# Performance work log

Hardware: AMD Instinct MI355X
Metric: run time of the kernel (lower is better)

The kernel has to match this reference:

```python
import jax, jax.numpy as jnp
import numpy as np


def gcn_conv(x, src, dst, norm, W, b, n_nodes):
    # PyG GCNConv: out[dst] = sum_edges norm * (x @ W)[src] + b
    h = x @ W                      # [N, F_out]
    msg = h[src] * norm[:, None]   # [E', F_out] gather + scale
    out = jax.ops.segment_sum(msg, dst, num_segments=n_nodes)
    return out + b


def _gcn_norm(edge_index, n_nodes):
    # add self loops, compute symmetric normalization deg^-1/2[src]*deg^-1/2[dst]
    loop = jnp.arange(n_nodes, dtype=edge_index.dtype)
    src = jnp.concatenate([edge_index[0], loop])
    dst = jnp.concatenate([edge_index[1], loop])
    deg = jnp.zeros((n_nodes,), jnp.float32).at[dst].add(1.0)
    dinv = jnp.where(deg > 0, jax.lax.rsqrt(deg), 0.0)
    norm = dinv[src] * dinv[dst]
    return src, dst, norm


def setup_inputs() -> dict:
    key = jax.random.key(0)
    ks = jax.random.split(key, 5)
    N, E, C_in, C_out = 50000, 800000, 128, 32
    H = 2 * C_out
    x = jax.random.normal(ks[0], (N, C_in), jnp.float32)
    edge_index = jax.random.randint(ks[1], (2, E), 0, N, jnp.int64)
    s1 = 1.0 / np.sqrt(C_in)
    s2 = 1.0 / np.sqrt(H)
    W1 = jax.random.uniform(ks[2], (C_in, H), jnp.float32, -s1, s1)
    b1 = jnp.zeros((H,), jnp.float32)
    W_mu = jax.random.uniform(ks[3], (H, C_out), jnp.float32, -s2, s2)
    b_mu = jnp.zeros((C_out,), jnp.float32)
    W_ls = jax.random.uniform(ks[4], (H, C_out), jnp.float32, -s2, s2)
    b_ls = jnp.zeros((C_out,), jnp.float32)
    return {"x": x, "edge_index": edge_index, "W1": W1, "b1": b1,
            "W_mu": W_mu, "b_mu": b_mu, "W_ls": W_ls, "b_ls": b_ls}


def reference(x, edge_index, W1, b1, W_mu, b_mu, W_ls, b_ls):
    n_nodes = x.shape[0]
    src, dst, norm = _gcn_norm(edge_index, n_nodes)
    h = jax.nn.relu(gcn_conv(x, src, dst, norm, W1, b1, n_nodes))
    mu = gcn_conv(h, src, dst, norm, W_mu, b_mu, n_nodes)
    logstd = gcn_conv(h, src, dst, norm, W_ls, b_ls, n_nodes)
    return mu, logstd
```

## Files before the change

kernel.cpp:

```cpp
#include <hip/hip_runtime.h>
#include <hip/hip_fp16.h>
#include <math.h>


typedef unsigned int uint;
typedef unsigned short ushort;
typedef __attribute__((ext_vector_type(8))) short short8;
typedef __attribute__((ext_vector_type(4))) float f32x4;

__device__ __forceinline__ ushort f2bf(float x) {
    uint u = __float_as_uint(x);
    u += 0x7fffu + ((u >> 16) & 1u);
    return (ushort)(u >> 16);
}
__device__ __forceinline__ float bf2f(ushort h) {
    return __uint_as_float((uint)h << 16);
}

__global__ __launch_bounds__(256) void k_hist(
        const int* __restrict__ dst, int* __restrict__ bcount, int E) {
    __shared__ int h[256];
    const int tid = threadIdx.x;
    h[tid] = 0;
    __syncthreads();
    const int base = blockIdx.x * 2048;
    #pragma unroll
    for (int k = 0; k < 8; ++k) {
        int i = base + k * 256 + tid;
        if (i < E) {
            int d = __builtin_nontemporal_load(dst + i);
            atomicAdd(&h[d >> 8], 1);
        }
    }
    __syncthreads();
    if (h[tid]) atomicAdd(&bcount[tid], h[tid]);
}

__global__ __launch_bounds__(256) void k_scatterA(
        const int* __restrict__ src, const int* __restrict__ dst,
        const int* __restrict__ bcount, int* __restrict__ bcursor,
        uint* __restrict__ recs, int E) {
    __shared__ int h[256];
    __shared__ int p[256];
    __shared__ int rb[256];
    const int tid = threadIdx.x;
    h[tid] = 0;
    __syncthreads();
    const int base = blockIdx.x * 2048;
    uint rec[8]; int rk[8];
    #pragma unroll
    for (int k = 0; k < 8; ++k) {
        int i = base + k * 256 + tid;
        if (i < E) {
            int s = __builtin_nontemporal_load(src + i);
            int d = __builtin_nontemporal_load(dst + i);
            int b = d >> 8;
            rec[k] = (uint)s | ((uint)(d & 255) << 16) | ((uint)b << 24);
            rk[k] = atomicAdd(&h[b], 1);
        }
    }
    int v = bcount[tid];
    p[tid] = v;
    __syncthreads();
    #pragma unroll
    for (int off = 1; off < 256; off <<= 1) {
        int x = (tid >= off) ? p[tid - off] : 0;
        __syncthreads();
        p[tid] += x;
        __syncthreads();
    }
    const int excl = p[tid] - v;
    const int hv = h[tid];
    rb[tid] = excl + (hv ? atomicAdd(&bcursor[tid], hv) : 0);
    __syncthreads();
    #pragma unroll
    for (int k = 0; k < 8; ++k) {
        int i = base + k * 256 + tid;
        if (i < E) recs[rb[rec[k] >> 24] + rk[k]] = rec[k];
    }
}

__global__ __launch_bounds__(256, 4) void k_phaseB(
        const uint* __restrict__ recs, const int* __restrict__ bcount,
        int* __restrict__ row_ptr, float* __restrict__ dinv,
        ushort* __restrict__ edges, int N, int E, int NBUCK) {
    __shared__ int h[256];
    __shared__ int p[256];
    __shared__ uint rstage[8192];
    const int tid = threadIdx.x;
    const int bx  = blockIdx.x;
    int v = bcount[tid];
    p[tid] = v;
    h[tid] = 0;
    __syncthreads();
    #pragma unroll
    for (int off = 1; off < 256; off <<= 1) {
        int x = (tid >= off) ? p[tid - off] : 0;
        __syncthreads();
        p[tid] += x;
        __syncthreads();
    }
    const int cnt = bcount[bx];
    const int bs  = p[bx] - cnt;
    const bool stg = (cnt <= 8192);
    for (int i = tid; i < cnt; i += 256) {
        uint r = recs[bs + i];
        if (stg) rstage[i] = r;
        atomicAdd(&h[(r >> 16) & 255], 1);
    }
    __syncthreads();
    v = h[tid];
    p[tid] = v;
    __syncthreads();
    #pragma unroll
    for (int off = 1; off < 256; off <<= 1) {
        int x = (tid >= off) ? p[tid - off] : 0;
        __syncthreads();
        p[tid] += x;
        __syncthreads();
    }
    const int excl = p[tid] - v;
    const int node = bx * 256 + tid;
    if (node < N) {
        row_ptr[node] = bs + excl;
        dinv[node] = rsqrtf((float)(v + 1));
    }
    if (bx == NBUCK - 1 && tid == 0) row_ptr[N] = E;
    h[tid] = excl;
    __syncthreads();
    for (int i = tid; i < cnt; i += 256) {
        uint r = stg ? rstage[i] : recs[bs + i];
        int pos = atomicAdd(&h[(r >> 16) & 255], 1);
        edges[bs + pos] = (ushort)(r & 0xffffu);
    }
}

__global__ __launch_bounds__(256, 4) void k_gemm(
        const float* __restrict__ x, const float* __restrict__ W1,
        const float* __restrict__ dinv, ushort* __restrict__ hp, int N) {
    const int tid = threadIdx.x;
    const int w = tid >> 6, l = tid & 63;
    const int m = l & 15, q = l >> 4;
    const int row0 = blockIdx.x * 64 + w * 16;
    const size_t arow = (size_t)min(row0 + m, N - 1);
    f32x4 acc0 = {0.f, 0.f, 0.f, 0.f}, acc1 = acc0, acc2 = acc0, acc3 = acc0;
    #pragma unroll
    for (int kc = 0; kc < 4; ++kc) {
        const int kofs = kc * 32 + q * 8;
        const float4* xr = (const float4*)(x + arow * 128 + kofs);
        float4 xa = xr[0], xb = xr[1];
        short8 a;
        a[0] = (short)f2bf(xa.x); a[1] = (short)f2bf(xa.y);
        a[2] = (short)f2bf(xa.z); a[3] = (short)f2bf(xa.w);
        a[4] = (short)f2bf(xb.x); a[5] = (short)f2bf(xb.y);
        a[6] = (short)f2bf(xb.z); a[7] = (short)f2bf(xb.w);
        short8 b0, b1, b2, b3;
        #pragma unroll
        for (int i = 0; i < 8; ++i) {
            const float* wk = W1 + (size_t)(kofs + i) * 64 + m;
            b0[i] = (short)f2bf(wk[0]);
            b1[i] = (short)f2bf(wk[16]);
            b2[i] = (short)f2bf(wk[32]);
            b3[i] = (short)f2bf(wk[48]);
        }
        acc0 = __builtin_amdgcn_mfma_f32_16x16x32_bf16(a, b0, acc0, 0, 0, 0);
        acc1 = __builtin_amdgcn_mfma_f32_16x16x32_bf16(a, b1, acc1, 0, 0, 0);
        acc2 = __builtin_amdgcn_mfma_f32_16x16x32_bf16(a, b2, acc2, 0, 0, 0);
        acc3 = __builtin_amdgcn_mfma_f32_16x16x32_bf16(a, b3, acc3, 0, 0, 0);
    }
    #pragma unroll
    for (int r = 0; r < 4; ++r) {
        int row = row0 + q * 4 + r;
        if (row >= N) continue;
        float dv = dinv[row];
        ushort* hr = hp + (size_t)row * 64 + m;
        hr[0]  = f2bf(acc0[r] * dv);
        hr[16] = f2bf(acc1[r] * dv);
        hr[32] = f2bf(acc2[r] * dv);
        hr[48] = f2bf(acc3[r] * dv);
    }
}

__device__ __forceinline__ f32x4 gather_grp(
        const uint* __restrict__ hp, const ushort* __restrict__ edges,
        int beg, int end, int E, int ql) {
    f32x4 acc = {0.f, 0.f, 0.f, 0.f};
    const int len = end - beg;
    int base = beg;
    for (int c = len >> 4; c > 0; --c, base += 16) {
        int mrec = (int)edges[base + ql];
        #pragma unroll
        for (int half = 0; half < 2; ++half) {
            #pragma unroll
            for (int i = 0; i < 8; ++i) {
                int r = __shfl(mrec, half * 8 + i, 16);
                uint2 v = *(const uint2*)(hp + (size_t)r * 32 + 2 * ql);
                f32x4 vf;
                vf.x = __uint_as_float(v.x << 16);
                vf.y = __uint_as_float(v.x & 0xffff0000u);
                vf.z = __uint_as_float(v.y << 16);
                vf.w = __uint_as_float(v.y & 0xffff0000u);
                acc = acc + vf;
            }
        }
    }
    const int rem = len & 15;
    if (rem) {
        int mrec = (int)edges[min(base + ql, E - 1)];
        for (int i = 0; i < rem; i += 4) {
            #pragma unroll
            for (int j = 0; j < 4; ++j) {
                int e = i + j;
                int r = __shfl(mrec, min(e, rem - 1), 16);
                uint2 v = *(const uint2*)(hp + (size_t)r * 32 + 2 * ql);
                if (e >= rem) { v.x = 0u; v.y = 0u; }
                f32x4 vf;
                vf.x = __uint_as_float(v.x << 16);
                vf.y = __uint_as_float(v.x & 0xffff0000u);
                vf.z = __uint_as_float(v.y << 16);
                vf.w = __uint_as_float(v.y & 0xffff0000u);
                acc = acc + vf;
            }
        }
    }
    return acc;
}

__global__ __launch_bounds__(256, 8) void k_gather1(
        const uint* __restrict__ hp, const int* __restrict__ row_ptr,
        const ushort* __restrict__ edges, const float* __restrict__ dinv,
        const float* __restrict__ b1, uint* __restrict__ ho, int N, int E) {
    const int lane = threadIdx.x & 63;
    const int ql = lane & 15;
    const int n = blockIdx.x * 16 + ((threadIdx.x >> 6) << 2) + (lane >> 4);
    const int nc = min(n, N - 1);
    const int beg = row_ptr[nc], end = row_ptr[nc + 1];
    f32x4 acc = gather_grp(hp, edges, beg, end, E, ql);
    const float dv = dinv[nc];
    const uint2 sv = *(const uint2*)(hp + (size_t)nc * 32 + 2 * ql);
    const float4 b = ((const float4*)b1)[ql];
    float s0 = acc.x + bf2f((ushort)sv.x);
    float s1 = acc.y + bf2f((ushort)(sv.x >> 16));
    float s2 = acc.z + bf2f((ushort)sv.y);
    float s3 = acc.w + bf2f((ushort)(sv.y >> 16));
    float h0 = fmaxf(fmaf(dv, s0, b.x), 0.f) * dv;
    float h1 = fmaxf(fmaf(dv, s1, b.y), 0.f) * dv;
    float h2 = fmaxf(fmaf(dv, s2, b.z), 0.f) * dv;
    float h3 = fmaxf(fmaf(dv, s3, b.w), 0.f) * dv;
    if (n < N) {
        uint2 o;
        o.x = (uint)f2bf(h0) | ((uint)f2bf(h1) << 16);
        o.y = (uint)f2bf(h2) | ((uint)f2bf(h3) << 16);
        *(uint2*)(ho + (size_t)n * 32 + 2 * ql) = o;
    }
}

__global__ __launch_bounds__(256, 8) void k_gather2(
        const uint* __restrict__ hp, const int* __restrict__ row_ptr,
        const ushort* __restrict__ edges, const float* __restrict__ dinv,
        const float* __restrict__ Wmu, const float* __restrict__ Wls,
        const float* __restrict__ bmu, const float* __restrict__ bls,
        float* __restrict__ out, int N, int E) {
    __shared__ __align__(16) float hs[4][4][64];
    const int lane = threadIdx.x & 63;
    const int ql = lane & 15, grp = lane >> 4;
    const int w = threadIdx.x >> 6;
    const int n = blockIdx.x * 16 + (w << 2) + grp;
    const int nc = min(n, N - 1);
    const int beg = row_ptr[nc], end = row_ptr[nc + 1];
    f32x4 acc = gather_grp(hp, edges, beg, end, E, ql);
    const float dv = dinv[nc];
    const uint2 sv = *(const uint2*)(hp + (size_t)nc * 32 + 2 * ql);
    float4 g;
    g.x = dv * (acc.x + bf2f((ushort)sv.x));
    g.y = dv * (acc.y + bf2f((ushort)(sv.x >> 16)));
    g.z = dv * (acc.z + bf2f((ushort)sv.y));
    g.w = dv * (acc.w + bf2f((ushort)(sv.y >> 16)));
    *(float4*)&hs[w][grp][4 * ql] = g;
    const float* Wsel = (lane < 32) ? (Wmu + lane) : (Wls + (lane - 32));
    const float bias  = (lane < 32) ? bmu[lane] : bls[lane - 32];
    float c0 = 0.f, c1 = 0.f, c2 = 0.f, c3 = 0.f;
    #pragma unroll 4
    for (int k = 0; k < 64; ++k) {
        float wv = Wsel[k * 32];
        c0 = fmaf(hs[w][0][k], wv, c0);
        c1 = fmaf(hs[w][1][k], wv, c1);
        c2 = fmaf(hs[w][2][k], wv, c2);
        c3 = fmaf(hs[w][3][k], wv, c3);
    }
    const int n0 = blockIdx.x * 16 + (w << 2);
    float cs[4] = {c0, c1, c2, c3};
    #pragma unroll
    for (int gg = 0; gg < 4; ++gg) {
        int nn = n0 + gg;
        if (nn >= N) break;
        float t = cs[gg] + bias;
        if (lane < 32) out[(size_t)nn * 32 + lane] = t;
        else           out[(size_t)N * 32 + (size_t)nn * 32 + (lane - 32)] = t;
    }
}

extern "C" void kernel_launch(void* const* d_in, const int* in_sizes, int n_in,
                              void* d_out, int out_size, void* d_ws, size_t ws_size,
                              hipStream_t stream) {
    const float* x   = (const float*)d_in[0];
    const int*   ei  = (const int*)d_in[1];
    const float* W1  = (const float*)d_in[2];
    const float* b1  = (const float*)d_in[3];
    const float* Wmu = (const float*)d_in[4];
    const float* bmu = (const float*)d_in[5];
    const float* Wls = (const float*)d_in[6];
    const float* bls = (const float*)d_in[7];
    float* out = (float*)d_out;

    const int N = in_sizes[0] / 128;
    const int E = in_sizes[1] / 2;
    const int* src = ei;
    const int* dst = ei + E;
    const int HB    = (E + 2047) / 2048;
    const int NBUCK = (N + 255) / 256;
    const int GB    = (N + 63) / 64;
    const int NG    = (N + 15) / 16;

    char* w = (char*)d_ws;
    auto carve = [&](size_t bytes) { char* p = w; w += (bytes + 1023) & ~(size_t)1023; return p; };
    int*    bcount  = (int*)   carve(512 * 4);
    int*    bcursor = bcount + 256;
    uint*   recs    = (uint*)  carve((size_t)E * 4);
    int*    row_ptr = (int*)   carve((size_t)(N + 1) * 4);
    float*  dinv    = (float*) carve((size_t)N * 4);
    ushort* edges   = (ushort*)carve((size_t)E * 2);
    ushort* h_pre   = (ushort*)carve((size_t)N * 64 * 2);
    ushort* h_mid   = (ushort*)carve((size_t)N * 64 * 2);

    hipMemsetAsync(bcount, 0, 512 * 4, stream);
    k_hist    <<<HB, 256, 0, stream>>>(dst, bcount, E);
    k_scatterA<<<HB, 256, 0, stream>>>(src, dst, bcount, bcursor, recs, E);
    k_phaseB  <<<NBUCK, 256, 0, stream>>>(recs, bcount, row_ptr, dinv, edges, N, E, NBUCK);
    k_gemm    <<<GB, 256, 0, stream>>>(x, W1, dinv, h_pre, N);
    k_gather1 <<<NG, 256, 0, stream>>>((const uint*)h_pre, row_ptr, edges, dinv,
                                       b1, (uint*)h_mid, N, E);
    k_gather2 <<<NG, 256, 0, stream>>>((const uint*)h_mid, row_ptr, edges, dinv,
                                       Wmu, Wls, bmu, bls, out, N, E);
}
```

Before: 188.8 us.

## Stage bf16 W1 in LDS for GEMM and gather with 8-lane groups using 16B loads

The GEMM kernel now converts W1 to bf16 once per block into a transposed shared-memory tile and reads B fragments as 16-byte LDS loads, instead of issuing many strided scalar global loads with per-element conversion. The gather kernels switch from 16 lanes per node with 8-byte loads to 8 lanes per node with 16-byte loads, so each wave handles 8 nodes and each block 32. Edge batches are 8 wide, with a masked tail of up to 7. The aim is fewer memory instructions per neighbour row and more nodes in flight, at the cost of more registers (occupancy hint lowered to 6) and extra GEMM prologue work.

```diff
diff --git a/kernel.cpp b/kernel.cpp
--- a/kernel.cpp
+++ b/kernel.cpp
@@ -138,7 +138,19 @@
 __global__ __launch_bounds__(256, 4) void k_gemm(
         const float* __restrict__ x, const float* __restrict__ W1,
         const float* __restrict__ dinv, ushort* __restrict__ hp, int N) {
+    __shared__ ushort Wt[64][136];
     const int tid = threadIdx.x;
+    #pragma unroll
+    for (int it = 0; it < 8; ++it) {
+        int idx = (it * 256 + tid) * 4;
+        int k = idx >> 6, c = idx & 63;
+        float4 wv = *(const float4*)(W1 + idx);
+        Wt[c + 0][k] = f2bf(wv.x);
+        Wt[c + 1][k] = f2bf(wv.y);
+        Wt[c + 2][k] = f2bf(wv.z);
+        Wt[c + 3][k] = f2bf(wv.w);
+    }
+    __syncthreads();
     const int w = tid >> 6, l = tid & 63;
     const int m = l & 15, q = l >> 4;
     const int row0 = blockIdx.x * 64 + w * 16;
@@ -154,15 +166,10 @@
         a[2] = (short)f2bf(xa.z); a[3] = (short)f2bf(xa.w);
         a[4] = (short)f2bf(xb.x); a[5] = (short)f2bf(xb.y);
         a[6] = (short)f2bf(xb.z); a[7] = (short)f2bf(xb.w);
-        short8 b0, b1, b2, b3;
-        #pragma unroll
-        for (int i = 0; i < 8; ++i) {
-            const float* wk = W1 + (size_t)(kofs + i) * 64 + m;
-            b0[i] = (short)f2bf(wk[0]);
-            b1[i] = (short)f2bf(wk[16]);
-            b2[i] = (short)f2bf(wk[32]);
-            b3[i] = (short)f2bf(wk[48]);
-        }
+        short8 b0 = *(const short8*)&Wt[m][kofs];
+        short8 b1 = *(const short8*)&Wt[m + 16][kofs];
+        short8 b2 = *(const short8*)&Wt[m + 32][kofs];
+        short8 b3 = *(const short8*)&Wt[m + 48][kofs];
         acc0 = __builtin_amdgcn_mfma_f32_16x16x32_bf16(a, b0, acc0, 0, 0, 0);
         acc1 = __builtin_amdgcn_mfma_f32_16x16x32_bf16(a, b1, acc1, 0, 0, 0);
         acc2 = __builtin_amdgcn_mfma_f32_16x16x32_bf16(a, b2, acc2, 0, 0, 0);
@@ -181,122 +188,137 @@
     }
 }
 
-__device__ __forceinline__ f32x4 gather_grp(
+__device__ __forceinline__ void gather_grp8(
         const uint* __restrict__ hp, const ushort* __restrict__ edges,
-        int beg, int end, int E, int ql) {
-    f32x4 acc = {0.f, 0.f, 0.f, 0.f};
-    const int len = end - beg;
-    int base = beg;
-    for (int c = len >> 4; c > 0; --c, base += 16) {
-        int mrec = (int)edges[base + ql];
-        #pragma unroll
-        for (int half = 0; half < 2; ++half) {
+        int beg, int end, int E, int sl, float4& a0, float4& a1) {
+    for (int base = beg; base < end; base += 8) {
+        const int mrec = (int)edges[min(base + sl, E - 1)];
+        const int cnt = end - base;
+        if (cnt >= 8) {
             #pragma unroll
             for (int i = 0; i < 8; ++i) {
-                int r = __shfl(mrec, half * 8 + i, 16);
-                uint2 v = *(const uint2*)(hp + (size_t)r * 32 + 2 * ql);
-                f32x4 vf;
-                vf.x = __uint_as_float(v.x << 16);
-                vf.y = __uint_as_float(v.x & 0xffff0000u);
-                vf.z = __uint_as_float(v.y << 16);
-                vf.w = __uint_as_float(v.y & 0xffff0000u);
-                acc = acc + vf;
+                const int r = __shfl(mrec, i, 8);
+                const uint4 v = *(const uint4*)(hp + (size_t)r * 32 + 4 * sl);
+                a0.x += __uint_as_float(v.x << 16);
+                a0.y += __uint_as_float(v.x & 0xffff0000u);
+                a0.z += __uint_as_float(v.y << 16);
+                a0.w += __uint_as_float(v.y & 0xffff0000u);
+                a1.x += __uint_as_float(v.z << 16);
+                a1.y += __uint_as_float(v.z & 0xffff0000u);
+                a1.z += __uint_as_float(v.w << 16);
+                a1.w += __uint_as_float(v.w & 0xffff0000u);
             }
-        }
-    }
-    const int rem = len & 15;
-    if (rem) {
-        int mrec = (int)edges[min(base + ql, E - 1)];
-        for (int i = 0; i < rem; i += 4) {
+        } else {
             #pragma unroll
-            for (int j = 0; j < 4; ++j) {
-                int e = i + j;
-                int r = __shfl(mrec, min(e, rem - 1), 16);
-                uint2 v = *(const uint2*)(hp + (size_t)r * 32 + 2 * ql);
-                if (e >= rem) { v.x = 0u; v.y = 0u; }
-                f32x4 vf;
-                vf.x = __uint_as_float(v.x << 16);
-                vf.y = __uint_as_float(v.x & 0xffff0000u);
-                vf.z = __uint_as_float(v.y << 16);
-                vf.w = __uint_as_float(v.y & 0xffff0000u);
-                acc = acc + vf;
+            for (int i = 0; i < 7; ++i) {
+                const int r = __shfl(mrec, min(i, cnt - 1), 8);
+                uint4 v = *(const uint4*)(hp + (size_t)r * 32 + 4 * sl);
+                if (i >= cnt) { v.x = 0u; v.y = 0u; v.z = 0u; v.w = 0u; }
+                a0.x += __uint_as_float(v.x << 16);
+                a0.y += __uint_as_float(v.x & 0xffff0000u);
+                a0.z += __uint_as_float(v.y << 16);
+                a0.w += __uint_as_float(v.y & 0xffff0000u);
+                a1.x += __uint_as_float(v.z << 16);
+                a1.y += __uint_as_float(v.z & 0xffff0000u);
+                a1.z += __uint_as_float(v.w << 16);
+                a1.w += __uint_as_float(v.w & 0xffff0000u);
             }
         }
     }
-    return acc;
-}
-
-__global__ __launch_bounds__(256, 8) void k_gather1(
+}
+
+__global__ __launch_bounds__(256, 6) void k_gather1(
         const uint* __restrict__ hp, const int* __restrict__ row_ptr,
         const ushort* __restrict__ edges, const float* __restrict__ dinv,
         const float* __restrict__ b1, uint* __restrict__ ho, int N, int E) {
     const int lane = threadIdx.x & 63;
-    const int ql = lane & 15;
-    const int n = blockIdx.x * 16 + ((threadIdx.x >> 6) << 2) + (lane >> 4);
+    const int sl = lane & 7;
+    const int n = blockIdx.x * 32 + ((threadIdx.x >> 6) << 3) + (lane >> 3);
     const int nc = min(n, N - 1);
     const int beg = row_ptr[nc], end = row_ptr[nc + 1];
-    f32x4 acc = gather_grp(hp, edges, beg, end, E, ql);
+    float4 a0 = {0.f, 0.f, 0.f, 0.f}, a1 = a0;
+    gather_grp8(hp, edges, beg, end, E, sl, a0, a1);
     const float dv = dinv[nc];
-    const uint2 sv = *(const uint2*)(hp + (size_t)nc * 32 + 2 * ql);
-    const float4 b = ((const float4*)b1)[ql];
-    float s0 = acc.x + bf2f((ushort)sv.x);
-    float s1 = acc.y + bf2f((ushort)(sv.x >> 16));
-    float s2 = acc.z + bf2f((ushort)sv.y);
-    float s3 = acc.w + bf2f((ushort)(sv.y >> 16));
-    float h0 = fmaxf(fmaf(dv, s0, b.x), 0.f) * dv;
-    float h1 = fmaxf(fmaf(dv, s1, b.y), 0.f) * dv;
-    float h2 = fmaxf(fmaf(dv, s2, b.z), 0.f) * dv;
-    float h3 = fmaxf(fmaf(dv, s3, b.w), 0.f) * dv;
+    const uint4 sv = *(const uint4*)(hp + (size_t)nc * 32 + 4 * sl);
+    const float4 bA = ((const float4*)b1)[2 * sl];
+    const float4 bB = ((const float4*)b1)[2 * sl + 1];
+    float s0 = a0.x + bf2f((ushort)sv.x);
+    float s1 = a0.y + bf2f((ushort)(sv.x >> 16));
+    float s2 = a0.z + bf2f((ushort)sv.y);
+    float s3 = a0.w + bf2f((ushort)(sv.y >> 16));
+    float s4 = a1.x + bf2f((ushort)sv.z);
+    float s5 = a1.y + bf2f((ushort)(sv.z >> 16));
+    float s6 = a1.z + bf2f((ushort)sv.w);
+    float s7 = a1.w + bf2f((ushort)(sv.w >> 16));
+    float h0 = fmaxf(fmaf(dv, s0, bA.x), 0.f) * dv;
+    float h1 = fmaxf(fmaf(dv, s1, bA.y), 0.f) * dv;
+    float h2 = fmaxf(fmaf(dv, s2, bA.z), 0.f) * dv;
+    float h3 = fmaxf(fmaf(dv, s3, bA.w), 0.f) * dv;
+    float h4 = fmaxf(fmaf(dv, s4, bB.x), 0.f) * dv;
+    float h5 = fmaxf(fmaf(dv, s5, bB.y), 0.f) * dv;
+    float h6 = fmaxf(fmaf(dv, s6, bB.z), 0.f) * dv;
+    float h7 = fmaxf(fmaf(dv, s7, bB.w), 0.f) * dv;
     if (n < N) {
-        uint2 o;
+        uint4 o;
         o.x = (uint)f2bf(h0) | ((uint)f2bf(h1) << 16);
         o.y = (uint)f2bf(h2) | ((uint)f2bf(h3) << 16);
-        *(uint2*)(ho + (size_t)n * 32 + 2 * ql) = o;
-    }
-}
-
-__global__ __launch_bounds__(256, 8) void k_gather2(
+        o.z = (uint)f2bf(h4) | ((uint)f2bf(h5) << 16);
+        o.w = (uint)f2bf(h6) | ((uint)f2bf(h7) << 16);
+        *(uint4*)(ho + (size_t)n * 32 + 4 * sl) = o;
+    }
+}
+
+__global__ __launch_bounds__(256, 6) void k_gather2(
         const uint* __restrict__ hp, const int* __restrict__ row_ptr,
         const ushort* __restrict__ edges, const float* __restrict__ dinv,
         const float* __restrict__ Wmu, const float* __restrict__ Wls,
         const float* __restrict__ bmu, const float* __restrict__ bls,
         float* __restrict__ out, int N, int E) {
-    __shared__ __align__(16) float hs[4][4][64];
+    __shared__ __align__(16) float hs[4][8][64];
     const int lane = threadIdx.x & 63;
-    const int ql = lane & 15, grp = lane >> 4;
+    const int sl = lane & 7, grp = lane >> 3;
     const int w = threadIdx.x >> 6;
-    const int n = blockIdx.x * 16 + (w << 2) + grp;
+    const int n = blockIdx.x * 32 + (w << 3) + grp;
     const int nc = min(n, N - 1);
     const int beg = row_ptr[nc], end = row_ptr[nc + 1];
-    f32x4 acc = gather_grp(hp, edges, beg, end, E, ql);
+    float4 a0 = {0.f, 0.f, 0.f, 0.f}, a1 = a0;
+    gather_grp8(hp, edges, beg, end, E, sl, a0, a1);
     const float dv = dinv[nc];
-    const uint2 sv = *(const uint2*)(hp + (size_t)nc * 32 + 2 * ql);
-    float4 g;
-    g.x = dv * (acc.x + bf2f((ushort)sv.x));
-    g.y = dv * (acc.y + bf2f((ushort)(sv.x >> 16)));
-    g.z = dv * (acc.z + bf2f((ushort)sv.y));
-    g.w = dv * (acc.w + bf2f((ushort)(sv.y >> 16)));
-    *(float4*)&hs[w][grp][4 * ql] = g;
+    const uint4 sv = *(const uint4*)(hp + (size_t)nc * 32 + 4 * sl);
+    float4 gA, gB;
+    gA.x = dv * (a0.x + bf2f((ushort)sv.x));
+    gA.y = dv * (a0.y + bf2f((ushort)(sv.x >> 16)));
+    gA.z = dv * (a0.z + bf2f((ushort)sv.y));
+    gA.w = dv * (a0.w + bf2f((ushort)(sv.y >> 16)));
+    gB.x = dv * (a1.x + bf2f((ushort)sv.z));
+    gB.y = dv * (a1.y + bf2f((ushort)(sv.z >> 16)));
+    gB.z = dv * (a1.z + bf2f((ushort)sv.w));
+    gB.w = dv * (a1.w + bf2f((ushort)(sv.w >> 16)));
+    *(float4*)&hs[w][grp][8 * sl]     = gA;
+    *(float4*)&hs[w][grp][8 * sl + 4] = gB;
     const float* Wsel = (lane < 32) ? (Wmu + lane) : (Wls + (lane - 32));
     const float bias  = (lane < 32) ? bmu[lane] : bls[lane - 32];
-    float c0 = 0.f, c1 = 0.f, c2 = 0.f, c3 = 0.f;
-    #pragma unroll 4
-    for (int k = 0; k < 64; ++k) {
-        float wv = Wsel[k * 32];
-        c0 = fmaf(hs[w][0][k], wv, c0);
-        c1 = fmaf(hs[w][1][k], wv, c1);
-        c2 = fmaf(hs[w][2][k], wv, c2);
-        c3 = fmaf(hs[w][3][k], wv, c3);
-    }
-    const int n0 = blockIdx.x * 16 + (w << 2);
-    float cs[4] = {c0, c1, c2, c3};
-    #pragma unroll
-    for (int gg = 0; gg < 4; ++gg) {
-        int nn = n0 + gg;
-        if (nn >= N) break;
-        float t = cs[gg] + bias;
-        if (lane < 32) out[(size_t)nn * 32 + lane] = t;
-        else           out[(size_t)N * 32 + (size_t)nn * 32 + (lane - 32)] = t;
+    #pragma unroll
+    for (int p = 0; p < 2; ++p) {
+        float c0 = 0.f, c1 = 0.f, c2 = 0.f, c3 = 0.f;
+        #pragma unroll 4
+        for (int k = 0; k < 64; ++k) {
+            float wv = Wsel[k * 32];
+            c0 = fmaf(hs[w][p * 4 + 0][k], wv, c0);
+            c1 = fmaf(hs[w][p * 4 + 1][k], wv, c1);
+            c2 = fmaf(hs[w][p * 4 + 2][k], wv, c2);
+            c3 = fmaf(hs[w][p * 4 + 3][k], wv, c3);
+        }
+        const int n0 = blockIdx.x * 32 + (w << 3) + p * 4;
+        float cs[4] = {c0, c1, c2, c3};
+        #pragma unroll
+        for (int gg = 0; gg < 4; ++gg) {
+            int nn = n0 + gg;
+            if (nn >= N) break;
+            float t = cs[gg] + bias;
+            if (lane < 32) out[(size_t)nn * 32 + lane] = t;
+            else           out[(size_t)N * 32 + (size_t)nn * 32 + (lane - 32)] = t;
+        }
     }
 }
 
@@ -320,7 +342,7 @@
     const int HB    = (E + 2047) / 2048;
     const int NBUCK = (N + 255) / 256;
     const int GB    = (N + 63) / 64;
-    const int NG    = (N + 15) / 16;
+    const int NG    = (N + 31) / 32;
 
     char* w = (char*)d_ws;
     auto carve = [&](size_t bytes) { char* p = w; w += (bytes + 1023) & ~(size_t)1023; return p; };
```

New measurement: 182.1 us. -3.5%, faster.
